# Kernel tuning notes

Hardware: AMD Instinct MI355X
Metric: run time of the kernel (lower is better)

Reference implementation:

```python
import jax, jax.numpy as jnp
import numpy as np

N_HEADS = 4
ROPE_THETA = 10000.0


def rotate_half(x):
    h = x.shape[-1] // 2
    return jnp.concatenate([-x[..., h:], x[..., :h]], axis=-1)


def setup_inputs() -> dict:
    key = jax.random.key(0)
    k1, k2, k3, k4, k5 = jax.random.split(key, 5)
    B, L, D, M = 4, 2048, 216, 64
    x = jax.random.normal(k1, (B, L, D), dtype=jnp.float32)
    mem_k = jax.random.normal(k2, (B, M, D), dtype=jnp.float32)
    mem_v = jax.random.normal(k3, (B, M, D), dtype=jnp.float32)
    attention_mask = jnp.ones((B, L), dtype=jnp.int32)
    # pre-transposed Linear weights (y = x @ W); scaled for stability
    Wqkv = jax.random.normal(k4, (D, 3 * D), dtype=jnp.float32) * (D ** -0.5)
    Wo = jax.random.normal(k5, (D, D), dtype=jnp.float32) * (D ** -0.5)
    return {"x": x, "mem_k": mem_k, "mem_v": mem_v,
            "attention_mask": attention_mask, "Wqkv": Wqkv, "Wo": Wo}


def reference(x, mem_k, mem_v, attention_mask, Wqkv, Wo):
    B, L, D = x.shape
    H = N_HEADS
    hd = D // H
    scale = hd ** -0.5
    M = mem_k.shape[1]

    # QKV projection -> [B, L, 3, H, hd] -> [B, H, L, hd]
    qkv = (x @ Wqkv).reshape(B, L, 3, H, hd)
    q = jnp.transpose(qkv[:, :, 0], (0, 2, 1, 3))
    k = jnp.transpose(qkv[:, :, 1], (0, 2, 1, 3))
    v = jnp.transpose(qkv[:, :, 2], (0, 2, 1, 3))

    # RoPE (cos/sin: [L, hd], broadcast over B,H)
    inv_freq = 1.0 / (ROPE_THETA ** (jnp.arange(0, hd, 2, dtype=jnp.float32) / hd))
    t = jnp.arange(L, dtype=jnp.float32)
    freqs = jnp.outer(t, inv_freq)
    emb = jnp.concatenate([freqs, freqs], axis=-1)
    cos, sin = jnp.cos(emb), jnp.sin(emb)
    q = q * cos + rotate_half(q) * sin
    k = k * cos + rotate_half(k) * sin

    # memory KV: [B, M, D] -> [B, H, M, hd], prepend along kv axis
    mk = jnp.transpose(mem_k.reshape(B, M, H, hd), (0, 2, 1, 3))
    mv = jnp.transpose(mem_v.reshape(B, M, H, hd), (0, 2, 1, 3))
    k_all = jnp.concatenate([mk, k], axis=2)  # [B, H, M+L, hd]
    v_all = jnp.concatenate([mv, v], axis=2)

    scores = jnp.einsum('bhld,bhmd->bhlm', q, k_all) * scale  # [B,H,L,M+L]

    # causal mask applies only to the self-attention block (cols >= M)
    causal = jnp.triu(jnp.ones((L, L), dtype=bool), k=1)
    full_causal = jnp.concatenate([jnp.zeros((L, M), dtype=bool), causal], axis=1)
    scores = jnp.where(full_causal[None, None], -jnp.inf, scores)

    # padding mask: memory positions always valid
    combined = jnp.concatenate(
        [jnp.ones((B, M), dtype=attention_mask.dtype), attention_mask], axis=-1)
    scores = jnp.where(combined[:, None, None, :] == 0, -jnp.inf, scores)

    attn = jax.nn.softmax(scores, axis=-1)  # dropout is identity in eval
    out = jnp.einsum('bhlm,bhmd->bhld', attn, v_all)
    out = jnp.transpose(out, (0, 2, 1, 3)).reshape(B, L, D)
    return out @ Wo
```

## Files before the change

kernel.cpp:

```cpp
#include <hip/hip_runtime.h>
#include <math.h>

#define B_ 4
#define L_ 2048
#define D_ 216
#define H_ 4
#define HD 54
#define HDP 64
#define M_ 64
#define LK 2112
#define NT_ 33
#define KP 256
#define SPB 84
#define QSCALE 0.19632593f

typedef __attribute__((ext_vector_type(8))) __bf16 bf16x8;
typedef __attribute__((ext_vector_type(4))) __bf16 bf16x4;
typedef __attribute__((ext_vector_type(4))) float f32x4;

__device__ __forceinline__ int unpack_d(int j) { return (j >> 1) + 27 * (j & 1); }

__global__ __launch_bounds__(256) void prep(const float* __restrict__ Wqkv,
                                            const float* __restrict__ Wo,
                                            const int* __restrict__ amask,
                                            const float* __restrict__ mk,
                                            const float* __restrict__ mv,
                                            __bf16* __restrict__ wqkvt,
                                            __bf16* __restrict__ wot,
                                            float2* __restrict__ table,
                                            float* __restrict__ bias,
                                            int* __restrict__ padflag,
                                            __bf16* __restrict__ kall,
                                            __bf16* __restrict__ vt) {
    const int bid = blockIdx.x, tid = threadIdx.x;
    if (bid < 768) {
        int idx = bid * 256 + tid;
        int pc = idx >> 8, k = idx & 255;
        float v = 0.f;
        if (k < 216) {
            int col = -1;
            if (pc < 256) { int h = pc >> 6, j = pc & 63;
                if (j < HD) col = h * HD + unpack_d(j); }
            else if (pc < 512) { int h = (pc - 256) >> 6, j = (pc - 256) & 63;
                if (j < HD) col = 216 + h * HD + unpack_d(j); }
            else if (pc < 728) col = 432 + (pc - 512);
            if (col >= 0) v = Wqkv[(size_t)k * 648 + col];
        }
        wqkvt[idx] = (__bf16)v;
    } else if (bid < 1024) {
        int idx = (bid - 768) * 256 + tid;
        int n = idx >> 8, k = idx & 255;
        wot[idx] = (__bf16)((n < 216 && k < 216) ? Wo[(size_t)k * 216 + n] : 0.f);
    } else if (bid < 1280) {
        int idx = (bid - 1024) * 256 + tid;
        int l = idx >> 5, ii = idx & 31;
        float2 sc = {0.f, 0.f};
        if (ii < 27) {
            float ang = (float)l * exp2f(-0.49213749924f * (float)ii);
            sc.x = sinf(ang); sc.y = cosf(ang);
        }
        table[idx] = sc;
    } else if (bid < 1313) {
        int idx = (bid - 1280) * 256 + tid;
        if (idx < B_ * LK) {
            int b = idx / LK, c = idx % LK;
            bias[idx] = (c < M_ || amask[b * L_ + c - M_] != 0) ? 0.f : -1e30f;
        }
    } else if (bid == 1313) {
        if (tid < B_ * NT_) {
            int b = tid / NT_, tile = tid % NT_;
            int flag = 0;
            for (int u = 0; u < 64; ++u) {
                int c = tile * 64 + u;
                if (c >= M_ && c < LK && amask[b * L_ + c - M_] == 0) flag = 1;
            }
            padflag[tid] = flag;
        }
    } else {
        int idx = (bid - 1314) * 256 + tid;
        int b  = idx >> 14;
        int m  = (idx >> 8) & 63;
        int h  = (idx >> 6) & 3;
        int dd = idx & 63;
        float kv = (dd < HD) ? mk[((size_t)(b * M_ + m)) * D_ + h * HD + unpack_d(dd)] : 0.f;
        kall[((size_t)(b * 4 + h) * LK + m) * HDP + dd] = (__bf16)kv;
        if (dd < HD)
            vt[((size_t)(b * 4 + h) * HD + dd) * LK + m] =
                (__bf16)mv[((size_t)(b * M_ + m)) * D_ + h * HD + dd];
    }
}

__global__ __launch_bounds__(256) void gemm_qkv(const float* __restrict__ x,
                                                const __bf16* __restrict__ Bt,
                                                const float2* __restrict__ table,
                                                __bf16* __restrict__ qb,
                                                __bf16* __restrict__ kall,
                                                __bf16* __restrict__ vt) {
    __shared__ __align__(16) __bf16 As[8192];
    __shared__ __align__(16) __bf16 Bs[4096];
    const int col0 = blockIdx.x * 64;
    const int row0 = blockIdx.y * 128;
    const int tid = threadIdx.x;
    const int lane = tid & 63;
    const int w = tid >> 6, wm = w >> 1, wn = w & 1;
    const int l15 = lane & 15, l4 = lane >> 4;

    f32x4 acc[4][2];
    #pragma unroll
    for (int m = 0; m < 4; ++m)
        #pragma unroll
        for (int n = 0; n < 2; ++n) acc[m][n] = (f32x4){0.f, 0.f, 0.f, 0.f};

    float4 rfa[4][2];
    bf16x8 rb[2];
    #pragma unroll
    for (int i = 0; i < 4; ++i) { int c = tid + 256 * i, r = c >> 3, c8 = c & 7;
        int k = c8 * 8;
        rfa[i][0] = *reinterpret_cast<const float4*>(x + (size_t)(row0 + r) * 216 + k);
        rfa[i][1] = *reinterpret_cast<const float4*>(x + (size_t)(row0 + r) * 216 + k + 4); }
    #pragma unroll
    for (int i = 0; i < 2; ++i) { int c = tid + 256 * i, r = c >> 3, c8 = c & 7;
        rb[i] = *reinterpret_cast<const bf16x8*>(Bt + (size_t)(col0 + r) * KP + c8 * 8); }

    for (int kit = 0; kit < 4; ++kit) {
        __syncthreads();
        #pragma unroll
        for (int i = 0; i < 4; ++i) { int c = tid + 256 * i, r = c >> 3, c8 = c & 7;
            bf16x8 v;
            #pragma unroll
            for (int j = 0; j < 4; ++j) { v[j] = (__bf16)rfa[i][0][j]; v[4 + j] = (__bf16)rfa[i][1][j]; }
            *reinterpret_cast<bf16x8*>(&As[r * 64 + ((c8 ^ (r & 7)) * 8)]) = v; }
        #pragma unroll
        for (int i = 0; i < 2; ++i) { int c = tid + 256 * i, r = c >> 3, c8 = c & 7;
            *reinterpret_cast<bf16x8*>(&Bs[r * 64 + ((c8 ^ (r & 7)) * 8)]) = rb[i]; }
        __syncthreads();
        if (kit < 3) {
            const int k0 = (kit + 1) * 64;
            #pragma unroll
            for (int i = 0; i < 4; ++i) { int c = tid + 256 * i, r = c >> 3, c8 = c & 7;
                int k = k0 + c8 * 8;
                if (k < 216) {
                    rfa[i][0] = *reinterpret_cast<const float4*>(x + (size_t)(row0 + r) * 216 + k);
                    rfa[i][1] = *reinterpret_cast<const float4*>(x + (size_t)(row0 + r) * 216 + k + 4);
                } else {
                    rfa[i][0] = (float4){0.f, 0.f, 0.f, 0.f};
                    rfa[i][1] = (float4){0.f, 0.f, 0.f, 0.f};
                } }
            #pragma unroll
            for (int i = 0; i < 2; ++i) { int c = tid + 256 * i, r = c >> 3, c8 = c & 7;
                rb[i] = *reinterpret_cast<const bf16x8*>(Bt + (size_t)(col0 + r) * KP + k0 + c8 * 8); }
        }
        #pragma unroll
        for (int ks = 0; ks < 2; ++ks) {
            bf16x8 af[4], bfr[2];
            #pragma unroll
            for (int m = 0; m < 4; ++m) { int row = wm * 64 + m * 16 + l15; int ch = ks * 4 + l4;
                af[m] = *reinterpret_cast<const bf16x8*>(&As[row * 64 + ((ch ^ (row & 7)) * 8)]); }
            #pragma unroll
            for (int n = 0; n < 2; ++n) { int row = wn * 32 + n * 16 + l15; int ch = ks * 4 + l4;
                bfr[n] = *reinterpret_cast<const bf16x8*>(&Bs[row * 64 + ((ch ^ (row & 7)) * 8)]); }
            #pragma unroll
            for (int m = 0; m < 4; ++m)
                #pragma unroll
                for (int n = 0; n < 2; ++n)
                    acc[m][n] = __builtin_amdgcn_mfma_f32_16x16x32_bf16(af[m], bfr[n], acc[m][n], 0, 0, 0);
        }
    }

    #pragma unroll
    for (int m = 0; m < 4; ++m)
        #pragma unroll
        for (int n = 0; n < 2; ++n) {
            const int cc = col0 + wn * 32 + n * 16 + l15;
            const int rowb = row0 + wm * 64 + m * 16 + l4 * 4;
            const int b = rowb >> 11;
            const int lbase = rowb & 2047;
            if (cc < 512) {
                const bool isq = cc < 256;
                const int h = (cc >> 6) & 3, j = cc & 63;
                const int half = j & 1, ii = j >> 1;
                #pragma unroll
                for (int rr = 0; rr < 4; ++rr) {
                    float me = acc[m][n][rr];
                    float pr = __shfl_xor(me, 1);
                    float2 sc = table[(lbase + rr) * 32 + ii];
                    float v = me * sc.y + (half ? pr * sc.x : -pr * sc.x);
                    if (isq) {
                        qb[((size_t)(b * 4 + h) * L_ + lbase + rr) * HDP + j] =
                            (__bf16)(v * QSCALE);
                    } else {
                        kall[((size_t)(b * 4 + h) * LK + M_ + lbase + rr) * HDP + j] =
                            (__bf16)v;
                    }
                }
            } else if (cc < 728) {
                const int dp = cc - 512;
                const int h = (dp * 1214) >> 16;
                const int d = dp - h * 54;
                #pragma unroll
                for (int rr = 0; rr < 4; ++rr)
                    vt[((size_t)(b * 4 + h) * HD + d) * LK + M_ + lbase + rr] =
                        (__bf16)acc[m][n][rr];
            }
        }
}

__global__ __launch_bounds__(256) void gemm_out(const __bf16* __restrict__ A,
                                                const __bf16* __restrict__ Bt,
                                                float* __restrict__ C, int N) {
    __shared__ __align__(16) __bf16 As[8192];
    __shared__ __align__(16) __bf16 Bs[4096];
    const int col0 = blockIdx.x * 64;
    const int row0 = blockIdx.y * 128;
    const int tid = threadIdx.x;
    const int lane = tid & 63;
    const int w = tid >> 6, wm = w >> 1, wn = w & 1;
    const int l15 = lane & 15, l4 = lane >> 4;

    f32x4 acc[4][2];
    #pragma unroll
    for (int m = 0; m < 4; ++m)
        #pragma unroll
        for (int n = 0; n < 2; ++n) acc[m][n] = (f32x4){0.f, 0.f, 0.f, 0.f};

    bf16x8 ra[4], rb[2];
    #pragma unroll
    for (int i = 0; i < 4; ++i) { int c = tid + 256 * i, r = c >> 3, c8 = c & 7;
        ra[i] = *reinterpret_cast<const bf16x8*>(A + (size_t)(row0 + r) * KP + c8 * 8); }
    #pragma unroll
    for (int i = 0; i < 2; ++i) { int c = tid + 256 * i, r = c >> 3, c8 = c & 7;
        rb[i] = *reinterpret_cast<const bf16x8*>(Bt + (size_t)(col0 + r) * KP + c8 * 8); }

    for (int kit = 0; kit < 4; ++kit) {
        __syncthreads();
        #pragma unroll
        for (int i = 0; i < 4; ++i) { int c = tid + 256 * i, r = c >> 3, c8 = c & 7;
            *reinterpret_cast<bf16x8*>(&As[r * 64 + ((c8 ^ (r & 7)) * 8)]) = ra[i]; }
        #pragma unroll
        for (int i = 0; i < 2; ++i) { int c = tid + 256 * i, r = c >> 3, c8 = c & 7;
            *reinterpret_cast<bf16x8*>(&Bs[r * 64 + ((c8 ^ (r & 7)) * 8)]) = rb[i]; }
        __syncthreads();
        if (kit < 3) {
            const int k0 = (kit + 1) * 64;
            #pragma unroll
            for (int i = 0; i < 4; ++i) { int c = tid + 256 * i, r = c >> 3, c8 = c & 7;
                ra[i] = *reinterpret_cast<const bf16x8*>(A + (size_t)(row0 + r) * KP + k0 + c8 * 8); }
            #pragma unroll
            for (int i = 0; i < 2; ++i) { int c = tid + 256 * i, r = c >> 3, c8 = c & 7;
                rb[i] = *reinterpret_cast<const bf16x8*>(Bt + (size_t)(col0 + r) * KP + k0 + c8 * 8); }
        }
        #pragma unroll
        for (int ks = 0; ks < 2; ++ks) {
            bf16x8 af[4], bfr[2];
            #pragma unroll
            for (int m = 0; m < 4; ++m) { int row = wm * 64 + m * 16 + l15; int ch = ks * 4 + l4;
                af[m] = *reinterpret_cast<const bf16x8*>(&As[row * 64 + ((ch ^ (row & 7)) * 8)]); }
            #pragma unroll
            for (int n = 0; n < 2; ++n) { int row = wn * 32 + n * 16 + l15; int ch = ks * 4 + l4;
                bfr[n] = *reinterpret_cast<const bf16x8*>(&Bs[row * 64 + ((ch ^ (row & 7)) * 8)]); }
            #pragma unroll
            for (int m = 0; m < 4; ++m)
                #pragma unroll
                for (int n = 0; n < 2; ++n)
                    acc[m][n] = __builtin_amdgcn_mfma_f32_16x16x32_bf16(af[m], bfr[n], acc[m][n], 0, 0, 0);
        }
    }
    #pragma unroll
    for (int m = 0; m < 4; ++m)
        #pragma unroll
        for (int n = 0; n < 2; ++n) {
            int cc = col0 + wn * 32 + n * 16 + l15;
            if (cc < N) {
                #pragma unroll
                for (int rr = 0; rr < 4; ++rr)
                    C[(size_t)(row0 + wm * 64 + m * 16 + l4 * 4 + rr) * N + cc] = acc[m][n][rr];
            }
        }
}

__global__ __launch_bounds__(256) void flash_split(const __bf16* __restrict__ qb,
                                                   const __bf16* __restrict__ kall,
                                                   const __bf16* __restrict__ vt,
                                                   const float* __restrict__ bias,
                                                   const int* __restrict__ padflag,
                                                   float* __restrict__ op,
                                                   float* __restrict__ ml) {
    int qt = 31, sp = 0;
    {
        int sidx = blockIdx.x, accq = 0;
        for (int q = 0; q < 32; ++q) {
            int c = (q + 9) >> 3;
            if (sidx < accq + c) { qt = q; sp = sidx - accq; break; }
            accq += c;
        }
    }
    const int pb = blockIdx.y * SPB + blockIdx.x;
    const int q0 = qt * 64;
    const int bh = blockIdx.y;
    const int b = bh >> 2;
    const int tstart = sp * 8;
    const int tend = min(tstart + 8, qt + 2);

    __shared__ __align__(16) __bf16 Qs[4096];
    __shared__ __align__(16) __bf16 Ks[4096];
    __shared__ __align__(16) __bf16 Vs[4096];
    __shared__ __align__(16) __bf16 Ps[4096];
    __shared__ float biasS[64];

    const int tid = threadIdx.x;
    const int lane = tid & 63;
    const int w = tid >> 6;
    const int l15 = lane & 15;
    const int l4 = lane >> 4;

    {
        const __bf16* src = qb + ((size_t)bh * L_ + q0) * HDP;
        for (int ch = tid; ch < 512; ch += 256) {
            int row = ch >> 3, c8 = ch & 7;
            bf16x8 v = *reinterpret_cast<const bf16x8*>(src + ch * 8);
            *reinterpret_cast<bf16x8*>(&Qs[row * 64 + ((c8 ^ (row & 7)) * 8)]) = v;
        }
        if (tid < 80) {
            int d = 54 + (tid >> 3), c8 = tid & 7;
            bf16x8 z{};
            *reinterpret_cast<bf16x8*>(&Vs[d * 64 + ((c8 ^ (d & 7)) * 8)]) = z;
        }
    }

    const int rq = q0 + 16 * w + l15;
    const __bf16* kbase = kall + (size_t)bh * LK * HDP;
    const __bf16* vbase = vt + (size_t)bh * HD * LK;

    bf16x8 rk[2], rv[2];
    float biasR = 0.f;
    int flagC;
    {
        const __bf16* ks = kbase + (size_t)tstart * 64 * HDP;
        rk[0] = *reinterpret_cast<const bf16x8*>(ks + tid * 8);
        rk[1] = *reinterpret_cast<const bf16x8*>(ks + (tid + 256) * 8);
        { int d = tid >> 3, c8 = tid & 7;
          rv[0] = *reinterpret_cast<const bf16x8*>(vbase + (size_t)d * LK + tstart * 64 + c8 * 8); }
        if (tid < 176) { int c = tid + 256, d = c >> 3, c8 = c & 7;
          rv[1] = *reinterpret_cast<const bf16x8*>(vbase + (size_t)d * LK + tstart * 64 + c8 * 8); }
        if (tid < 64) biasR = bias[b * LK + tstart * 64 + tid];
        flagC = padflag[b * NT_ + tstart];
    }

    __syncthreads();
    bf16x8 aQ[2];
    {
        int qrow = 16 * w + l15, s = (qrow & 7) << 3;
        aQ[0] = *reinterpret_cast<const bf16x8*>(&Qs[qrow * 64 + ((l4 * 8) ^ s)]);
        aQ[1] = *reinterpret_cast<const bf16x8*>(&Qs[qrow * 64 + ((32 + l4 * 8) ^ s)]);
    }

    f32x4 Oacc[4];
    #pragma unroll
    for (int nt = 0; nt < 4; ++nt) Oacc[nt] = (f32x4){0.f, 0.f, 0.f, 0.f};
    float m_run = -1e30f, l_run = 0.f;

    for (int t = tstart; t < tend; ++t) {
        const int cbase = t * 64;
        __syncthreads();
        { int r = tid >> 3, c8 = tid & 7;
          *reinterpret_cast<bf16x8*>(&Ks[r * 64 + ((c8 ^ (r & 7)) * 8)]) = rk[0]; }
        { int c = tid + 256, r = c >> 3, c8 = c & 7;
          *reinterpret_cast<bf16x8*>(&Ks[r * 64 + ((c8 ^ (r & 7)) * 8)]) = rk[1]; }
        { int d = tid >> 3, c8 = tid & 7;
          *reinterpret_cast<bf16x8*>(&Vs[d * 64 + ((c8 ^ (d & 7)) * 8)]) = rv[0]; }
        if (tid < 176) { int c = tid + 256, d = c >> 3, c8 = c & 7;
          *reinterpret_cast<bf16x8*>(&Vs[d * 64 + ((c8 ^ (d & 7)) * 8)]) = rv[1]; }
        if (tid < 64) biasS[tid] = biasR;
        const int flag = flagC;
        __syncthreads();
        if (t + 1 < tend) {
            const __bf16* ks = kbase + (size_t)(cbase + 64) * HDP;
            rk[0] = *reinterpret_cast<const bf16x8*>(ks + tid * 8);
            rk[1] = *reinterpret_cast<const bf16x8*>(ks + (tid + 256) * 8);
            { int d = tid >> 3, c8 = tid & 7;
              rv[0] = *reinterpret_cast<const bf16x8*>(vbase + (size_t)d * LK + cbase + 64 + c8 * 8); }
            if (tid < 176) { int c = tid + 256, d = c >> 3, c8 = c & 7;
              rv[1] = *reinterpret_cast<const bf16x8*>(vbase + (size_t)d * LK + cbase + 64 + c8 * 8); }
            if (tid < 64) biasR = bias[b * LK + cbase + 64 + tid];
            flagC = padflag[b * NT_ + t + 1];
        }

        f32x4 S[4];
        #pragma unroll
        for (int nt = 0; nt < 4; ++nt) {
            int krow = nt * 16 + l15, s = (krow & 7) << 3;
            bf16x8 b0 = *reinterpret_cast<const bf16x8*>(&Ks[krow * 64 + ((l4 * 8) ^ s)]);
            bf16x8 b1 = *reinterpret_cast<const bf16x8*>(&Ks[krow * 64 + ((32 + l4 * 8) ^ s)]);
            f32x4 acc = (f32x4){0.f, 0.f, 0.f, 0.f};
            acc = __builtin_amdgcn_mfma_f32_16x16x32_bf16(b0, aQ[0], acc, 0, 0, 0);
            acc = __builtin_amdgcn_mfma_f32_16x16x32_bf16(b1, aQ[1], acc, 0, 0, 0);
            S[nt] = acc;
        }
        if (flag) {
            #pragma unroll
            for (int nt = 0; nt < 4; ++nt)
                #pragma unroll
                for (int r = 0; r < 4; ++r)
                    S[nt][r] += biasS[nt * 16 + l4 * 4 + r];
        }
        if (t == qt + 1) {
            #pragma unroll
            for (int nt = 0; nt < 4; ++nt)
                #pragma unroll
                for (int r = 0; r < 4; ++r) {
                    int cg = cbase + nt * 16 + l4 * 4 + r;
                    if (cg > rq + M_) S[nt][r] = -1e30f;
                }
        }
        float mx = fmaxf(fmaxf(S[0][0], S[0][1]), fmaxf(S[0][2], S[0][3]));
        #pragma unroll
        for (int nt = 1; nt < 4; ++nt)
            mx = fmaxf(mx, fmaxf(fmaxf(S[nt][0], S[nt][1]), fmaxf(S[nt][2], S[nt][3])));
        mx = fmaxf(mx, __shfl_xor(mx, 16));
        mx = fmaxf(mx, __shfl_xor(mx, 32));
        float m_new = fmaxf(m_run, mx);
        float alpha = exp2f(m_run - m_new);
        m_run = m_new;
        float ls = 0.f;
        #pragma unroll
        for (int nt = 0; nt < 4; ++nt)
            #pragma unroll
            for (int r = 0; r < 4; ++r) {
                float p = exp2f(S[nt][r] - m_new);
                S[nt][r] = p;
                ls += p;
            }
        ls += __shfl_xor(ls, 16);
        ls += __shfl_xor(ls, 32);
        l_run = l_run * alpha + ls;
        {
            int prow = 16 * w + l15, s = (prow & 7) << 3;
            #pragma unroll
            for (int nt = 0; nt < 4; ++nt) {
                bf16x4 pk;
                pk[0] = (__bf16)S[nt][0]; pk[1] = (__bf16)S[nt][1];
                pk[2] = (__bf16)S[nt][2]; pk[3] = (__bf16)S[nt][3];
                *reinterpret_cast<bf16x4*>(&Ps[prow * 64 + ((nt * 16 + l4 * 4) ^ s)]) = pk;
            }
        }
        float aO[4];
        #pragma unroll
        for (int r = 0; r < 4; ++r)
            aO[r] = __shfl(alpha, (lane & 0x30) | (l4 * 4 + r), 64);
        #pragma unroll
        for (int nt = 0; nt < 4; ++nt)
            #pragma unroll
            for (int r = 0; r < 4; ++r) Oacc[nt][r] *= aO[r];
        bf16x8 aP[2];
        {
            int prow = 16 * w + l15, s = (prow & 7) << 3;
            aP[0] = *reinterpret_cast<const bf16x8*>(&Ps[prow * 64 + ((l4 * 8) ^ s)]);
            aP[1] = *reinterpret_cast<const bf16x8*>(&Ps[prow * 64 + ((32 + l4 * 8) ^ s)]);
        }
        #pragma unroll
        for (int nt = 0; nt < 4; ++nt) {
            int vrow = nt * 16 + l15, s = (vrow & 7) << 3;
            bf16x8 v0 = *reinterpret_cast<const bf16x8*>(&Vs[vrow * 64 + ((l4 * 8) ^ s)]);
            bf16x8 v1 = *reinterpret_cast<const bf16x8*>(&Vs[vrow * 64 + ((32 + l4 * 8) ^ s)]);
            Oacc[nt] = __builtin_amdgcn_mfma_f32_16x16x32_bf16(aP[0], v0, Oacc[nt], 0, 0, 0);
            Oacc[nt] = __builtin_amdgcn_mfma_f32_16x16x32_bf16(aP[1], v1, Oacc[nt], 0, 0, 0);
        }
    }

    if (l4 == 0) {
        ml[((size_t)pb * 64 + 16 * w + l15) * 2 + 0] = m_run;
        ml[((size_t)pb * 64 + 16 * w + l15) * 2 + 1] = l_run;
    }
    #pragma unroll
    for (int nt = 0; nt < 4; ++nt) {
        int c = nt * 16 + l15;
        if (c < HD) {
            #pragma unroll
            for (int r = 0; r < 4; ++r)
                op[((size_t)pb * HD + c) * 64 + 16 * w + l4 * 4 + r] = Oacc[nt][r];
        }
    }
}

__global__ __launch_bounds__(256) void combine(const float* __restrict__ op,
                                               const float* __restrict__ ml,
                                               __bf16* __restrict__ aoutb) {
    const int qt = blockIdx.x, bh = blockIdx.y;
    const int b = bh >> 2, h = bh & 3;
    const int ns = (qt + 9) >> 3;
    int accq = 0;
    for (int q = 0; q < qt; ++q) accq += (q + 9) >> 3;
    const int pb0 = bh * SPB + accq;
    const int row = threadIdx.x & 63;
    const int dseg = threadIdx.x >> 6;

    float mi[5], li[5];
    float m = -1e30f;
    for (int i = 0; i < ns; ++i) {
        mi[i] = ml[((size_t)(pb0 + i) * 64 + row) * 2 + 0];
        li[i] = ml[((size_t)(pb0 + i) * 64 + row) * 2 + 1];
        m = fmaxf(m, mi[i]);
    }
    float wgt[5], Lr = 0.f;
    for (int i = 0; i < ns; ++i) {
        wgt[i] = exp2f(mi[i] - m);
        Lr += li[i] * wgt[i];
    }
    float inv = 1.f / Lr;
    #pragma unroll
    for (int j = 0; j < 14; ++j) {
        int d = dseg * 14 + j;
        if (d < HD) {
            float o = 0.f;
            for (int i = 0; i < ns; ++i)
                o += wgt[i] * op[((size_t)(pb0 + i) * HD + d) * 64 + row];
            aoutb[((size_t)(b * L_) + qt * 64 + row) * KP + h * HD + d] = (__bf16)(o * inv);
        }
    }
}

extern "C" void kernel_launch(void* const* d_in, const int* in_sizes, int n_in,
                              void* d_out, int out_size, void* d_ws, size_t ws_size,
                              hipStream_t stream) {
    const float* x     = (const float*)d_in[0];
    const float* mem_k = (const float*)d_in[1];
    const float* mem_v = (const float*)d_in[2];
    const int*   amask = (const int*)d_in[3];
    const float* Wqkv  = (const float*)d_in[4];
    const float* Wo    = (const float*)d_in[5];
    float* out = (float*)d_out;

    char* p = (char*)d_ws;
    float* bias    = (float*)p;        p += (size_t)B_ * LK * 4;
    int*   padflag = (int*)p;          p += (size_t)B_ * NT_ * 4;
    float2* table  = (float2*)p;       p += (size_t)2048 * 32 * 8;
    __bf16* wqkvt  = (__bf16*)p;       p += (size_t)768 * KP * 2;
    __bf16* wot    = (__bf16*)p;       p += (size_t)256 * KP * 2;
    __bf16* aoutb  = (__bf16*)p;       p += (size_t)8192 * KP * 2;
    __bf16* qb     = (__bf16*)p;       p += (size_t)16 * 2048 * 64 * 2;
    __bf16* kall   = (__bf16*)p;       p += (size_t)16 * 2112 * 64 * 2;
    __bf16* vt     = (__bf16*)p;       p += (size_t)16 * 54 * 2112 * 2;
    float* opbuf   = (float*)p;        p += (size_t)16 * SPB * HD * 64 * 4;
    float* mlbuf   = (float*)p;        p += (size_t)16 * SPB * 64 * 2 * 4;

    prep<<<dim3(1570), 256, 0, stream>>>(Wqkv, Wo, amask, mem_k, mem_v,
                                         wqkvt, wot, table, bias, padflag, kall, vt);
    gemm_qkv<<<dim3(12, 64), 256, 0, stream>>>(x, wqkvt, table, qb, kall, vt);
    flash_split<<<dim3(SPB, 16), 256, 0, stream>>>(qb, kall, vt, bias, padflag,
                                                   opbuf, mlbuf);
    combine<<<dim3(32, 16), 256, 0, stream>>>(opbuf, mlbuf, aoutb);
    gemm_out<<<dim3(4, 64), 256, 0, stream>>>(aoutb, wot, out, 216);
}
```

Baseline: 99.71 us.

## Enlarge flash attention query tile to 128 rows with two row groups per wave

Doubles the query tile per block from 64 to 128 rows, so each wave handles two 16-row groups that share each loaded K/V tile. This halves the K/V global loads and LDS staging per query row and cuts the number of split blocks. The split indexing, causal masking range, partial-output layout and combine kernel are updated to match. In exchange it uses more registers and LDS and launches fewer blocks (44x16 instead of 84x16), which may lower occupancy and add causal-diagonal waste.

```diff
diff --git a/kernel.cpp b/kernel.cpp
--- a/kernel.cpp
+++ b/kernel.cpp
@@ -11,7 +11,8 @@
 #define LK 2112
 #define NT_ 33
 #define KP 256
-#define SPB 84
+#define QT_ 16
+#define SPB 44
 #define QSCALE 0.19632593f
 
 typedef __attribute__((ext_vector_type(8))) __bf16 bf16x8;
@@ -285,26 +286,27 @@
                                                    const int* __restrict__ padflag,
                                                    float* __restrict__ op,
                                                    float* __restrict__ ml) {
-    int qt = 31, sp = 0;
+    int qt = QT_ - 1, sp = 0;
     {
         int sidx = blockIdx.x, accq = 0;
-        for (int q = 0; q < 32; ++q) {
-            int c = (q + 9) >> 3;
+        for (int q = 0; q < QT_; ++q) {
+            int c = (2 * q + 10) >> 3;
             if (sidx < accq + c) { qt = q; sp = sidx - accq; break; }
             accq += c;
         }
     }
     const int pb = blockIdx.y * SPB + blockIdx.x;
-    const int q0 = qt * 64;
+    const int q0 = qt * 128;
     const int bh = blockIdx.y;
     const int b = bh >> 2;
+    const int ktiles = 2 * qt + 3;
     const int tstart = sp * 8;
-    const int tend = min(tstart + 8, qt + 2);
-
-    __shared__ __align__(16) __bf16 Qs[4096];
+    const int tend = min(tstart + 8, ktiles);
+
+    __shared__ __align__(16) __bf16 Qs[8192];
     __shared__ __align__(16) __bf16 Ks[4096];
     __shared__ __align__(16) __bf16 Vs[4096];
-    __shared__ __align__(16) __bf16 Ps[4096];
+    __shared__ __align__(16) __bf16 Ps[8192];
     __shared__ float biasS[64];
 
     const int tid = threadIdx.x;
@@ -315,7 +317,7 @@
 
     {
         const __bf16* src = qb + ((size_t)bh * L_ + q0) * HDP;
-        for (int ch = tid; ch < 512; ch += 256) {
+        for (int ch = tid; ch < 1024; ch += 256) {
             int row = ch >> 3, c8 = ch & 7;
             bf16x8 v = *reinterpret_cast<const bf16x8*>(src + ch * 8);
             *reinterpret_cast<bf16x8*>(&Qs[row * 64 + ((c8 ^ (row & 7)) * 8)]) = v;
@@ -327,7 +329,6 @@
         }
     }
 
-    const int rq = q0 + 16 * w + l15;
     const __bf16* kbase = kall + (size_t)bh * LK * HDP;
     const __bf16* vbase = vt + (size_t)bh * HD * LK;
 
@@ -347,17 +348,22 @@
     }
 
     __syncthreads();
-    bf16x8 aQ[2];
-    {
-        int qrow = 16 * w + l15, s = (qrow & 7) << 3;
-        aQ[0] = *reinterpret_cast<const bf16x8*>(&Qs[qrow * 64 + ((l4 * 8) ^ s)]);
-        aQ[1] = *reinterpret_cast<const bf16x8*>(&Qs[qrow * 64 + ((32 + l4 * 8) ^ s)]);
-    }
-
-    f32x4 Oacc[4];
-    #pragma unroll
-    for (int nt = 0; nt < 4; ++nt) Oacc[nt] = (f32x4){0.f, 0.f, 0.f, 0.f};
-    float m_run = -1e30f, l_run = 0.f;
+    bf16x8 aQ[2][2];
+    #pragma unroll
+    for (int g = 0; g < 2; ++g) {
+        int qrow = 32 * w + 16 * g + l15, s = (qrow & 7) << 3;
+        aQ[g][0] = *reinterpret_cast<const bf16x8*>(&Qs[qrow * 64 + ((l4 * 8) ^ s)]);
+        aQ[g][1] = *reinterpret_cast<const bf16x8*>(&Qs[qrow * 64 + ((32 + l4 * 8) ^ s)]);
+    }
+
+    f32x4 Oacc[2][4];
+    float m_run[2], l_run[2];
+    #pragma unroll
+    for (int g = 0; g < 2; ++g) {
+        m_run[g] = -1e30f; l_run[g] = 0.f;
+        #pragma unroll
+        for (int nt = 0; nt < 4; ++nt) Oacc[g][nt] = (f32x4){0.f, 0.f, 0.f, 0.f};
+    }
 
     for (int t = tstart; t < tend; ++t) {
         const int cbase = t * 64;
@@ -385,101 +391,127 @@
             flagC = padflag[b * NT_ + t + 1];
         }
 
-        f32x4 S[4];
+        f32x4 S[2][4];
         #pragma unroll
         for (int nt = 0; nt < 4; ++nt) {
             int krow = nt * 16 + l15, s = (krow & 7) << 3;
             bf16x8 b0 = *reinterpret_cast<const bf16x8*>(&Ks[krow * 64 + ((l4 * 8) ^ s)]);
             bf16x8 b1 = *reinterpret_cast<const bf16x8*>(&Ks[krow * 64 + ((32 + l4 * 8) ^ s)]);
-            f32x4 acc = (f32x4){0.f, 0.f, 0.f, 0.f};
-            acc = __builtin_amdgcn_mfma_f32_16x16x32_bf16(b0, aQ[0], acc, 0, 0, 0);
-            acc = __builtin_amdgcn_mfma_f32_16x16x32_bf16(b1, aQ[1], acc, 0, 0, 0);
-            S[nt] = acc;
+            #pragma unroll
+            for (int g = 0; g < 2; ++g) {
+                f32x4 acc = (f32x4){0.f, 0.f, 0.f, 0.f};
+                acc = __builtin_amdgcn_mfma_f32_16x16x32_bf16(b0, aQ[g][0], acc, 0, 0, 0);
+                acc = __builtin_amdgcn_mfma_f32_16x16x32_bf16(b1, aQ[g][1], acc, 0, 0, 0);
+                S[g][nt] = acc;
+            }
         }
         if (flag) {
             #pragma unroll
+            for (int g = 0; g < 2; ++g)
+                #pragma unroll
+                for (int nt = 0; nt < 4; ++nt)
+                    #pragma unroll
+                    for (int r = 0; r < 4; ++r)
+                        S[g][nt][r] += biasS[nt * 16 + l4 * 4 + r];
+        }
+        if (t >= 2 * qt + 1) {
+            #pragma unroll
+            for (int g = 0; g < 2; ++g) {
+                int rq = q0 + 32 * w + 16 * g + l15;
+                #pragma unroll
+                for (int nt = 0; nt < 4; ++nt)
+                    #pragma unroll
+                    for (int r = 0; r < 4; ++r) {
+                        int cg = cbase + nt * 16 + l4 * 4 + r;
+                        if (cg > rq + M_) S[g][nt][r] = -1e30f;
+                    }
+            }
+        }
+        float alpha[2];
+        #pragma unroll
+        for (int g = 0; g < 2; ++g) {
+            float mx = fmaxf(fmaxf(S[g][0][0], S[g][0][1]), fmaxf(S[g][0][2], S[g][0][3]));
+            #pragma unroll
+            for (int nt = 1; nt < 4; ++nt)
+                mx = fmaxf(mx, fmaxf(fmaxf(S[g][nt][0], S[g][nt][1]),
+                                     fmaxf(S[g][nt][2], S[g][nt][3])));
+            mx = fmaxf(mx, __shfl_xor(mx, 16));
+            mx = fmaxf(mx, __shfl_xor(mx, 32));
+            float m_new = fmaxf(m_run[g], mx);
+            alpha[g] = exp2f(m_run[g] - m_new);
+            m_run[g] = m_new;
+            float ls = 0.f;
+            #pragma unroll
             for (int nt = 0; nt < 4; ++nt)
                 #pragma unroll
-                for (int r = 0; r < 4; ++r)
-                    S[nt][r] += biasS[nt * 16 + l4 * 4 + r];
-        }
-        if (t == qt + 1) {
-            #pragma unroll
-            for (int nt = 0; nt < 4; ++nt)
-                #pragma unroll
                 for (int r = 0; r < 4; ++r) {
-                    int cg = cbase + nt * 16 + l4 * 4 + r;
-                    if (cg > rq + M_) S[nt][r] = -1e30f;
+                    float pv = exp2f(S[g][nt][r] - m_new);
+                    S[g][nt][r] = pv;
+                    ls += pv;
                 }
-        }
-        float mx = fmaxf(fmaxf(S[0][0], S[0][1]), fmaxf(S[0][2], S[0][3]));
-        #pragma unroll
-        for (int nt = 1; nt < 4; ++nt)
-            mx = fmaxf(mx, fmaxf(fmaxf(S[nt][0], S[nt][1]), fmaxf(S[nt][2], S[nt][3])));
-        mx = fmaxf(mx, __shfl_xor(mx, 16));
-        mx = fmaxf(mx, __shfl_xor(mx, 32));
-        float m_new = fmaxf(m_run, mx);
-        float alpha = exp2f(m_run - m_new);
-        m_run = m_new;
-        float ls = 0.f;
-        #pragma unroll
-        for (int nt = 0; nt < 4; ++nt)
-            #pragma unroll
-            for (int r = 0; r < 4; ++r) {
-                float p = exp2f(S[nt][r] - m_new);
-                S[nt][r] = p;
-                ls += p;
-            }
-        ls += __shfl_xor(ls, 16);
-        ls += __shfl_xor(ls, 32);
-        l_run = l_run * alpha + ls;
-        {
-            int prow = 16 * w + l15, s = (prow & 7) << 3;
+            ls += __shfl_xor(ls, 16);
+            ls += __shfl_xor(ls, 32);
+            l_run[g] = l_run[g] * alpha[g] + ls;
+            int prow = 32 * w + 16 * g + l15, s = (prow & 7) << 3;
             #pragma unroll
             for (int nt = 0; nt < 4; ++nt) {
                 bf16x4 pk;
-                pk[0] = (__bf16)S[nt][0]; pk[1] = (__bf16)S[nt][1];
-                pk[2] = (__bf16)S[nt][2]; pk[3] = (__bf16)S[nt][3];
+                pk[0] = (__bf16)S[g][nt][0]; pk[1] = (__bf16)S[g][nt][1];
+                pk[2] = (__bf16)S[g][nt][2]; pk[3] = (__bf16)S[g][nt][3];
                 *reinterpret_cast<bf16x4*>(&Ps[prow * 64 + ((nt * 16 + l4 * 4) ^ s)]) = pk;
             }
         }
-        float aO[4];
-        #pragma unroll
-        for (int r = 0; r < 4; ++r)
-            aO[r] = __shfl(alpha, (lane & 0x30) | (l4 * 4 + r), 64);
-        #pragma unroll
-        for (int nt = 0; nt < 4; ++nt)
-            #pragma unroll
-            for (int r = 0; r < 4; ++r) Oacc[nt][r] *= aO[r];
-        bf16x8 aP[2];
-        {
-            int prow = 16 * w + l15, s = (prow & 7) << 3;
-            aP[0] = *reinterpret_cast<const bf16x8*>(&Ps[prow * 64 + ((l4 * 8) ^ s)]);
-            aP[1] = *reinterpret_cast<const bf16x8*>(&Ps[prow * 64 + ((32 + l4 * 8) ^ s)]);
+        #pragma unroll
+        for (int g = 0; g < 2; ++g) {
+            float aO[4];
+            #pragma unroll
+            for (int r = 0; r < 4; ++r)
+                aO[r] = __shfl(alpha[g], (lane & 0x30) | (l4 * 4 + r), 64);
+            #pragma unroll
+            for (int nt = 0; nt < 4; ++nt)
+                #pragma unroll
+                for (int r = 0; r < 4; ++r) Oacc[g][nt][r] *= aO[r];
+        }
+        bf16x8 aP[2][2];
+        #pragma unroll
+        for (int g = 0; g < 2; ++g) {
+            int prow = 32 * w + 16 * g + l15, s = (prow & 7) << 3;
+            aP[g][0] = *reinterpret_cast<const bf16x8*>(&Ps[prow * 64 + ((l4 * 8) ^ s)]);
+            aP[g][1] = *reinterpret_cast<const bf16x8*>(&Ps[prow * 64 + ((32 + l4 * 8) ^ s)]);
         }
         #pragma unroll
         for (int nt = 0; nt < 4; ++nt) {
             int vrow = nt * 16 + l15, s = (vrow & 7) << 3;
             bf16x8 v0 = *reinterpret_cast<const bf16x8*>(&Vs[vrow * 64 + ((l4 * 8) ^ s)]);
             bf16x8 v1 = *reinterpret_cast<const bf16x8*>(&Vs[vrow * 64 + ((32 + l4 * 8) ^ s)]);
-            Oacc[nt] = __builtin_amdgcn_mfma_f32_16x16x32_bf16(aP[0], v0, Oacc[nt], 0, 0, 0);
-            Oacc[nt] = __builtin_amdgcn_mfma_f32_16x16x32_bf16(aP[1], v1, Oacc[nt], 0, 0, 0);
+            #pragma unroll
+            for (int g = 0; g < 2; ++g) {
+                Oacc[g][nt] = __builtin_amdgcn_mfma_f32_16x16x32_bf16(aP[g][0], v0, Oacc[g][nt], 0, 0, 0);
+                Oacc[g][nt] = __builtin_amdgcn_mfma_f32_16x16x32_bf16(aP[g][1], v1, Oacc[g][nt], 0, 0, 0);
+            }
         }
     }
 
     if (l4 == 0) {
-        ml[((size_t)pb * 64 + 16 * w + l15) * 2 + 0] = m_run;
-        ml[((size_t)pb * 64 + 16 * w + l15) * 2 + 1] = l_run;
-    }
-    #pragma unroll
-    for (int nt = 0; nt < 4; ++nt) {
-        int c = nt * 16 + l15;
-        if (c < HD) {
-            #pragma unroll
-            for (int r = 0; r < 4; ++r)
-                op[((size_t)pb * HD + c) * 64 + 16 * w + l4 * 4 + r] = Oacc[nt][r];
-        }
-    }
+        #pragma unroll
+        for (int g = 0; g < 2; ++g) {
+            int row = 32 * w + 16 * g + l15;
+            ml[((size_t)pb * 128 + row) * 2 + 0] = m_run[g];
+            ml[((size_t)pb * 128 + row) * 2 + 1] = l_run[g];
+        }
+    }
+    #pragma unroll
+    for (int g = 0; g < 2; ++g)
+        #pragma unroll
+        for (int nt = 0; nt < 4; ++nt) {
+            int c = nt * 16 + l15;
+            if (c < HD) {
+                #pragma unroll
+                for (int r = 0; r < 4; ++r)
+                    op[((size_t)pb * HD + c) * 128 + 32 * w + 16 * g + l4 * 4 + r] =
+                        Oacc[g][nt][r];
+            }
+        }
 }
 
 __global__ __launch_bounds__(256) void combine(const float* __restrict__ op,
@@ -487,18 +519,18 @@
                                                __bf16* __restrict__ aoutb) {
     const int qt = blockIdx.x, bh = blockIdx.y;
     const int b = bh >> 2, h = bh & 3;
-    const int ns = (qt + 9) >> 3;
+    const int ns = (2 * qt + 10) >> 3;
     int accq = 0;
-    for (int q = 0; q < qt; ++q) accq += (q + 9) >> 3;
+    for (int q = 0; q < qt; ++q) accq += (2 * q + 10) >> 3;
     const int pb0 = bh * SPB + accq;
-    const int row = threadIdx.x & 63;
-    const int dseg = threadIdx.x >> 6;
+    const int row = threadIdx.x & 127;
+    const int dseg = threadIdx.x >> 7;
 
     float mi[5], li[5];
     float m = -1e30f;
     for (int i = 0; i < ns; ++i) {
-        mi[i] = ml[((size_t)(pb0 + i) * 64 + row) * 2 + 0];
-        li[i] = ml[((size_t)(pb0 + i) * 64 + row) * 2 + 1];
+        mi[i] = ml[((size_t)(pb0 + i) * 128 + row) * 2 + 0];
+        li[i] = ml[((size_t)(pb0 + i) * 128 + row) * 2 + 1];
         m = fmaxf(m, mi[i]);
     }
     float wgt[5], Lr = 0.f;
@@ -508,14 +540,12 @@
     }
     float inv = 1.f / Lr;
     #pragma unroll
-    for (int j = 0; j < 14; ++j) {
-        int d = dseg * 14 + j;
-        if (d < HD) {
-            float o = 0.f;
-            for (int i = 0; i < ns; ++i)
-                o += wgt[i] * op[((size_t)(pb0 + i) * HD + d) * 64 + row];
-            aoutb[((size_t)(b * L_) + qt * 64 + row) * KP + h * HD + d] = (__bf16)(o * inv);
-        }
+    for (int j = 0; j < 27; ++j) {
+        int d = dseg * 27 + j;
+        float o = 0.f;
+        for (int i = 0; i < ns; ++i)
+            o += wgt[i] * op[((size_t)(pb0 + i) * HD + d) * 128 + row];
+        aoutb[((size_t)(b * L_) + qt * 128 + row) * KP + h * HD + d] = (__bf16)(o * inv);
     }
 }
 
@@ -540,14 +570,14 @@
     __bf16* qb     = (__bf16*)p;       p += (size_t)16 * 2048 * 64 * 2;
     __bf16* kall   = (__bf16*)p;       p += (size_t)16 * 2112 * 64 * 2;
     __bf16* vt     = (__bf16*)p;       p += (size_t)16 * 54 * 2112 * 2;
-    float* opbuf   = (float*)p;        p += (size_t)16 * SPB * HD * 64 * 4;
-    float* mlbuf   = (float*)p;        p += (size_t)16 * SPB * 64 * 2 * 4;
+    float* opbuf   = (float*)p;        p += (size_t)16 * SPB * HD * 128 * 4;
+    float* mlbuf   = (float*)p;        p += (size_t)16 * SPB * 128 * 2 * 4;
 
     prep<<<dim3(1570), 256, 0, stream>>>(Wqkv, Wo, amask, mem_k, mem_v,
                                          wqkvt, wot, table, bias, padflag, kall, vt);
     gemm_qkv<<<dim3(12, 64), 256, 0, stream>>>(x, wqkvt, table, qb, kall, vt);
     flash_split<<<dim3(SPB, 16), 256, 0, stream>>>(qb, kall, vt, bias, padflag,
                                                    opbuf, mlbuf);
-    combine<<<dim3(32, 16), 256, 0, stream>>>(opbuf, mlbuf, aoutb);
+    combine<<<dim3(QT_, 16), 256, 0, stream>>>(opbuf, mlbuf, aoutb);
     gemm_out<<<dim3(4, 64), 256, 0, stream>>>(aoutb, wot, out, 216);
 }
```

Result: slower. 123.5 us (+23.9%).

## Double-buffer K/V shared tiles to drop one barrier per iteration

Applied to the files above, without the earlier changes.

The attention split kernel now keeps two shared-memory buffers for K, V and bias. The next tile is written into the alternate buffer while the current one is consumed, and loads are prefetched two tiles ahead. This cuts the loop to one __syncthreads per iteration and overlaps the shared-memory stores with compute. It roughly doubles LDS use for K/V, which may lower occupancy, and the padflag is now read from global memory on each iteration.

```diff
diff --git a/kernel.cpp b/kernel.cpp
--- a/kernel.cpp
+++ b/kernel.cpp
@@ -302,10 +302,10 @@
     const int tend = min(tstart + 8, qt + 2);
 
     __shared__ __align__(16) __bf16 Qs[4096];
-    __shared__ __align__(16) __bf16 Ks[4096];
-    __shared__ __align__(16) __bf16 Vs[4096];
+    __shared__ __align__(16) __bf16 Ks[2][4096];
+    __shared__ __align__(16) __bf16 Vs[2][4096];
     __shared__ __align__(16) __bf16 Ps[4096];
-    __shared__ float biasS[64];
+    __shared__ float biasS[2][64];
 
     const int tid = threadIdx.x;
     const int lane = tid & 63;
@@ -320,10 +320,11 @@
             bf16x8 v = *reinterpret_cast<const bf16x8*>(src + ch * 8);
             *reinterpret_cast<bf16x8*>(&Qs[row * 64 + ((c8 ^ (row & 7)) * 8)]) = v;
         }
-        if (tid < 80) {
-            int d = 54 + (tid >> 3), c8 = tid & 7;
+        if (tid < 160) {
+            int buf = tid >= 80, q = tid - 80 * buf;
+            int d = 54 + (q >> 3), c8 = q & 7;
             bf16x8 z{};
-            *reinterpret_cast<bf16x8*>(&Vs[d * 64 + ((c8 ^ (d & 7)) * 8)]) = z;
+            *reinterpret_cast<bf16x8*>(&Vs[buf][d * 64 + ((c8 ^ (d & 7)) * 8)]) = z;
         }
     }
 
@@ -333,7 +334,6 @@
 
     bf16x8 rk[2], rv[2];
     float biasR = 0.f;
-    int flagC;
     {
         const __bf16* ks = kbase + (size_t)tstart * 64 * HDP;
         rk[0] = *reinterpret_cast<const bf16x8*>(ks + tid * 8);
@@ -343,7 +343,26 @@
         if (tid < 176) { int c = tid + 256, d = c >> 3, c8 = c & 7;
           rv[1] = *reinterpret_cast<const bf16x8*>(vbase + (size_t)d * LK + tstart * 64 + c8 * 8); }
         if (tid < 64) biasR = bias[b * LK + tstart * 64 + tid];
-        flagC = padflag[b * NT_ + tstart];
+
+        { int r = tid >> 3, c8 = tid & 7;
+          *reinterpret_cast<bf16x8*>(&Ks[0][r * 64 + ((c8 ^ (r & 7)) * 8)]) = rk[0]; }
+        { int c = tid + 256, r = c >> 3, c8 = c & 7;
+          *reinterpret_cast<bf16x8*>(&Ks[0][r * 64 + ((c8 ^ (r & 7)) * 8)]) = rk[1]; }
+        { int d = tid >> 3, c8 = tid & 7;
+          *reinterpret_cast<bf16x8*>(&Vs[0][d * 64 + ((c8 ^ (d & 7)) * 8)]) = rv[0]; }
+        if (tid < 176) { int c = tid + 256, d = c >> 3, c8 = c & 7;
+          *reinterpret_cast<bf16x8*>(&Vs[0][d * 64 + ((c8 ^ (d & 7)) * 8)]) = rv[1]; }
+        if (tid < 64) biasS[0][tid] = biasR;
+    }
+    if (tstart + 1 < tend) {
+        const __bf16* ks = kbase + (size_t)(tstart + 1) * 64 * HDP;
+        rk[0] = *reinterpret_cast<const bf16x8*>(ks + tid * 8);
+        rk[1] = *reinterpret_cast<const bf16x8*>(ks + (tid + 256) * 8);
+        { int d = tid >> 3, c8 = tid & 7;
+          rv[0] = *reinterpret_cast<const bf16x8*>(vbase + (size_t)d * LK + (tstart + 1) * 64 + c8 * 8); }
+        if (tid < 176) { int c = tid + 256, d = c >> 3, c8 = c & 7;
+          rv[1] = *reinterpret_cast<const bf16x8*>(vbase + (size_t)d * LK + (tstart + 1) * 64 + c8 * 8); }
+        if (tid < 64) biasR = bias[b * LK + (tstart + 1) * 64 + tid];
     }
 
     __syncthreads();
@@ -359,38 +378,39 @@
     for (int nt = 0; nt < 4; ++nt) Oacc[nt] = (f32x4){0.f, 0.f, 0.f, 0.f};
     float m_run = -1e30f, l_run = 0.f;
 
+    int p = 0;
     for (int t = tstart; t < tend; ++t) {
         const int cbase = t * 64;
-        __syncthreads();
-        { int r = tid >> 3, c8 = tid & 7;
-          *reinterpret_cast<bf16x8*>(&Ks[r * 64 + ((c8 ^ (r & 7)) * 8)]) = rk[0]; }
-        { int c = tid + 256, r = c >> 3, c8 = c & 7;
-          *reinterpret_cast<bf16x8*>(&Ks[r * 64 + ((c8 ^ (r & 7)) * 8)]) = rk[1]; }
-        { int d = tid >> 3, c8 = tid & 7;
-          *reinterpret_cast<bf16x8*>(&Vs[d * 64 + ((c8 ^ (d & 7)) * 8)]) = rv[0]; }
-        if (tid < 176) { int c = tid + 256, d = c >> 3, c8 = c & 7;
-          *reinterpret_cast<bf16x8*>(&Vs[d * 64 + ((c8 ^ (d & 7)) * 8)]) = rv[1]; }
-        if (tid < 64) biasS[tid] = biasR;
-        const int flag = flagC;
-        __syncthreads();
+        const int qbuf = p ^ 1;
         if (t + 1 < tend) {
-            const __bf16* ks = kbase + (size_t)(cbase + 64) * HDP;
+            { int r = tid >> 3, c8 = tid & 7;
+              *reinterpret_cast<bf16x8*>(&Ks[qbuf][r * 64 + ((c8 ^ (r & 7)) * 8)]) = rk[0]; }
+            { int c = tid + 256, r = c >> 3, c8 = c & 7;
+              *reinterpret_cast<bf16x8*>(&Ks[qbuf][r * 64 + ((c8 ^ (r & 7)) * 8)]) = rk[1]; }
+            { int d = tid >> 3, c8 = tid & 7;
+              *reinterpret_cast<bf16x8*>(&Vs[qbuf][d * 64 + ((c8 ^ (d & 7)) * 8)]) = rv[0]; }
+            if (tid < 176) { int c = tid + 256, d = c >> 3, c8 = c & 7;
+              *reinterpret_cast<bf16x8*>(&Vs[qbuf][d * 64 + ((c8 ^ (d & 7)) * 8)]) = rv[1]; }
+            if (tid < 64) biasS[qbuf][tid] = biasR;
+        }
+        if (t + 2 < tend) {
+            const __bf16* ks = kbase + (size_t)(cbase + 128) * HDP;
             rk[0] = *reinterpret_cast<const bf16x8*>(ks + tid * 8);
             rk[1] = *reinterpret_cast<const bf16x8*>(ks + (tid + 256) * 8);
             { int d = tid >> 3, c8 = tid & 7;
-              rv[0] = *reinterpret_cast<const bf16x8*>(vbase + (size_t)d * LK + cbase + 64 + c8 * 8); }
+              rv[0] = *reinterpret_cast<const bf16x8*>(vbase + (size_t)d * LK + cbase + 128 + c8 * 8); }
             if (tid < 176) { int c = tid + 256, d = c >> 3, c8 = c & 7;
-              rv[1] = *reinterpret_cast<const bf16x8*>(vbase + (size_t)d * LK + cbase + 64 + c8 * 8); }
-            if (tid < 64) biasR = bias[b * LK + cbase + 64 + tid];
-            flagC = padflag[b * NT_ + t + 1];
-        }
+              rv[1] = *reinterpret_cast<const bf16x8*>(vbase + (size_t)d * LK + cbase + 128 + c8 * 8); }
+            if (tid < 64) biasR = bias[b * LK + cbase + 128 + tid];
+        }
+        const int flag = padflag[b * NT_ + t];
 
         f32x4 S[4];
         #pragma unroll
         for (int nt = 0; nt < 4; ++nt) {
             int krow = nt * 16 + l15, s = (krow & 7) << 3;
-            bf16x8 b0 = *reinterpret_cast<const bf16x8*>(&Ks[krow * 64 + ((l4 * 8) ^ s)]);
-            bf16x8 b1 = *reinterpret_cast<const bf16x8*>(&Ks[krow * 64 + ((32 + l4 * 8) ^ s)]);
+            bf16x8 b0 = *reinterpret_cast<const bf16x8*>(&Ks[p][krow * 64 + ((l4 * 8) ^ s)]);
+            bf16x8 b1 = *reinterpret_cast<const bf16x8*>(&Ks[p][krow * 64 + ((32 + l4 * 8) ^ s)]);
             f32x4 acc = (f32x4){0.f, 0.f, 0.f, 0.f};
             acc = __builtin_amdgcn_mfma_f32_16x16x32_bf16(b0, aQ[0], acc, 0, 0, 0);
             acc = __builtin_amdgcn_mfma_f32_16x16x32_bf16(b1, aQ[1], acc, 0, 0, 0);
@@ -401,7 +421,7 @@
             for (int nt = 0; nt < 4; ++nt)
                 #pragma unroll
                 for (int r = 0; r < 4; ++r)
-                    S[nt][r] += biasS[nt * 16 + l4 * 4 + r];
+                    S[nt][r] += biasS[p][nt * 16 + l4 * 4 + r];
         }
         if (t == qt + 1) {
             #pragma unroll
@@ -426,9 +446,9 @@
         for (int nt = 0; nt < 4; ++nt)
             #pragma unroll
             for (int r = 0; r < 4; ++r) {
-                float p = exp2f(S[nt][r] - m_new);
-                S[nt][r] = p;
-                ls += p;
+                float pv = exp2f(S[nt][r] - m_new);
+                S[nt][r] = pv;
+                ls += pv;
             }
         ls += __shfl_xor(ls, 16);
         ls += __shfl_xor(ls, 32);
@@ -460,11 +480,13 @@
         #pragma unroll
         for (int nt = 0; nt < 4; ++nt) {
             int vrow = nt * 16 + l15, s = (vrow & 7) << 3;
-            bf16x8 v0 = *reinterpret_cast<const bf16x8*>(&Vs[vrow * 64 + ((l4 * 8) ^ s)]);
-            bf16x8 v1 = *reinterpret_cast<const bf16x8*>(&Vs[vrow * 64 + ((32 + l4 * 8) ^ s)]);
+            bf16x8 v0 = *reinterpret_cast<const bf16x8*>(&Vs[p][vrow * 64 + ((l4 * 8) ^ s)]);
+            bf16x8 v1 = *reinterpret_cast<const bf16x8*>(&Vs[p][vrow * 64 + ((32 + l4 * 8) ^ s)]);
             Oacc[nt] = __builtin_amdgcn_mfma_f32_16x16x32_bf16(aP[0], v0, Oacc[nt], 0, 0, 0);
             Oacc[nt] = __builtin_amdgcn_mfma_f32_16x16x32_bf16(aP[1], v1, Oacc[nt], 0, 0, 0);
         }
+        __syncthreads();
+        p ^= 1;
     }
 
     if (l4 == 0) {
```

New measurement: 100.7 us. About the same (+1.0%).
